# Performance work log

Hardware: AMD Instinct MI355X
Metric: run time of the kernel (lower is better)

Reference implementation:

```python
import jax, jax.numpy as jnp
import numpy as np

GROUP_SIZE = 128
INTERMEDIATE = 18944


def _unpack_int4(packed):
    # packed: [rows, cols//8] int32, 8 nibbles per int32 along output dim
    shifts = jnp.arange(8, dtype=jnp.int32) * 4
    nib = (packed[:, :, None] >> shifts) & 15  # [rows, cols//8, 8]
    return nib.reshape(packed.shape[0], packed.shape[1] * 8)


def awq_gemm(x, qweight, qzeros, scales, group_size):
    # Dequantize: W[i,j] = (w4[i,j] - z4[i//g, j]) * scales[i//g, j]
    w = _unpack_int4(qweight).astype(jnp.float32)           # [in, out]
    z = _unpack_int4(qzeros).astype(jnp.float32)            # [in//g, out]
    s = scales.astype(jnp.float32)                          # [in//g, out]
    W = ((w - jnp.repeat(z, group_size, axis=0)) * jnp.repeat(s, group_size, axis=0))
    return (x @ W.astype(x.dtype))                          # [tokens, out]


def setup_inputs() -> dict:
    key = jax.random.key(0)
    ks = jax.random.split(key, 7)
    imax = 2147483647
    return {
        "x": (jax.random.normal(ks[0], (4096, 3584), dtype=jnp.float32) * 0.02).astype(jnp.float16),
        "qweight_gu": jax.random.randint(ks[1], (3584, 4736), 0, imax, dtype=jnp.int32),
        "qzeros_gu": jax.random.randint(ks[2], (28, 4736), 0, imax, dtype=jnp.int32),
        "scales_gu": (jax.random.uniform(ks[3], (28, 37888), dtype=jnp.float32) * 0.01 + 0.001).astype(jnp.float16),
        "qweight_down": jax.random.randint(ks[4], (18944, 448), 0, imax, dtype=jnp.int32),
        "qzeros_down": jax.random.randint(ks[5], (148, 448), 0, imax, dtype=jnp.int32),
        "scales_down": (jax.random.uniform(ks[6], (148, 3584), dtype=jnp.float32) * 0.01 + 0.001).astype(jnp.float16),
    }


def reference(x, qweight_gu, qzeros_gu, scales_gu, qweight_down, qzeros_down, scales_down):
    # Fused gate+up AWQ GEMM (matches forward path after fuse_gate_up())
    gate_up = awq_gemm(x, qweight_gu, qzeros_gu, scales_gu, GROUP_SIZE)  # [T, 2*I]
    gate = gate_up[..., :INTERMEDIATE]
    up = gate_up[..., INTERMEDIATE:]
    intermediate = jax.nn.silu(gate) * up                                # fused SiLU*mul
    down = awq_gemm(intermediate, qweight_down, qzeros_down, scales_down, GROUP_SIZE)
    return down
```

## Files before the change

kernel.cpp:

```cpp
#include <hip/hip_runtime.h>
#include <hip/hip_fp16.h>
#include <stdint.h>

typedef _Float16 half8 __attribute__((ext_vector_type(8)));
typedef _Float16 h2v __attribute__((ext_vector_type(2)));
typedef float f32x4 __attribute__((ext_vector_type(4)));

#define GLD_LDS16(gp, lp)                                                     \
  __builtin_amdgcn_global_load_lds(                                           \
      (const __attribute__((address_space(1))) void*)(gp),                    \
      (__attribute__((address_space(3))) void*)(lp), 16, 0, 0)
#define GLD_LDS4(gp, lp)                                                      \
  __builtin_amdgcn_global_load_lds(                                           \
      (const __attribute__((address_space(1))) void*)(gp),                    \
      (__attribute__((address_space(3))) void*)(lp), 4, 0, 0)

__global__ void xcvt_kernel(const float* __restrict__ in, __half* __restrict__ out) {
  const size_t i = ((size_t)blockIdx.x * 256 + threadIdx.x) * 4;
  float4 v = *(const float4*)(in + i);
  __half2* o = (__half2*)(out + i);
  o[0] = __floats2half2_rn(v.x, v.y);
  o[1] = __floats2half2_rn(v.z, v.w);
}

__global__ void repack_kernel(const int* __restrict__ qw, uint32_t* __restrict__ rp, int P) {
  const int N = P * 8;
  const int n = blockIdx.x * 256 + threadIdx.x;
  const int j8 = n >> 3;
  const int sh = (n & 7) * 4;
  #pragma unroll
  for (int qi = 0; qi < 4; ++qi) {
    const int q = blockIdx.y * 4 + qi;
    const int* src = qw + (size_t)(q * 8) * P + j8;
    uint32_t r = 0;
    #pragma unroll
    for (int t = 0; t < 8; ++t) {
      uint32_t w = ((uint32_t)src[t * P] >> sh) & 15u;
      r |= w << (4 * (t >> 1) + 16 * (t & 1));
    }
    rp[(size_t)q * N + n] = r;
  }
}

__global__ void smz_kernel(const float* __restrict__ sc, const int* __restrict__ qz,
                           uint32_t* __restrict__ smz, int P) {
  const int N = P * 8;
  const int n = blockIdx.x * 256 + threadIdx.x;
  const int g = blockIdx.y;
  uint32_t sbits = __half_as_ushort(__float2half(sc[(size_t)g * N + n]));
  uint32_t z = ((uint32_t)qz[(size_t)g * P + (n >> 3)] >> ((n & 7) * 4)) & 15u;
  uint32_t hz = 0x6400u | z;
  smz[(size_t)g * N + n] = sbits | (hz << 16);
}

union U32H2 { uint32_t u; h2v h; };
__device__ inline h2v bith2(uint32_t u) { U32H2 t; t.u = u; return t.h; }
__device__ inline uint32_t h2bit(h2v h) { U32H2 t; t.h = h; return t.u; }
__device__ inline half8 dequant8(uint32_t p, h2v s, h2v z) {
  union { uint32_t u[4]; half8 v; } r;
  r.u[0] = h2bit((bith2((p & 0x000F000Fu) | 0x64006400u) - z) * s);
  r.u[1] = h2bit((bith2(((p >> 4) & 0x000F000Fu) | 0x64006400u) - z) * s);
  r.u[2] = h2bit((bith2(((p >> 8) & 0x000F000Fu) | 0x64006400u) - z) * s);
  r.u[3] = h2bit((bith2(((p >> 12) & 0x000F000Fu) | 0x64006400u) - z) * s);
  return r.v;
}

template <int KDIM, int NW, int T1OFF, int OW, bool SILU, int BXS>
__global__ __launch_bounds__(512, 2) void awq_gemm_big(const __half* __restrict__ A,
                                                       const uint32_t* __restrict__ RP,
                                                       const uint32_t* __restrict__ SMZ,
                                                       void* __restrict__ OUT) {
  constexpr int ABUF = 256 * 64 * 2;
  constexpr int BBUF = 8 * 256 * 4;
  constexpr int BOFF = 3 * ABUF;
  constexpr int ZOFF = BOFF + 3 * BBUF;
  __shared__ __align__(16) unsigned char smem[ZOFF + 2048];

  const int tid = threadIdx.x;
  const int l = tid & 63;
  const int wv = tid >> 6;
  const int wm = wv >> 2;
  const int wn = wv & 3;
  const int l15 = l & 15;
  const int l4 = l >> 4;
  const int l157 = l15 & 7;

  const int row0 = blockIdx.y * 256;
  const int n0 = blockIdx.x * BXS;

  const __half* asrc[4];
  #pragma unroll
  for (int it = 0; it < 4; ++it) {
    int m = it * 64 + (tid >> 3);
    int cs = tid & 7;
    int kc = cs ^ (m & 7);
    asrc[it] = A + (size_t)(row0 + m) * KDIM + kc * 8;
  }

  const uint32_t* bsrc;
  {
    int qr = tid >> 6;
    int c4 = (tid & 63) * 4;
    int S = ((qr & 1) << 4) | ((qr >> 1) << 2);
    int cS = c4 ^ S;
    int bcol = (cS < 128) ? n0 + cS : n0 + T1OFF + (cS - 128);
    bsrc = RP + (size_t)qr * NW + bcol;
  }

  const uint32_t* zsrc;
  {
    int zc = tid & 255;
    zsrc = SMZ + ((zc < 128) ? n0 + zc : n0 + T1OFF + (zc - 128));
  }

  int chi[4];
  #pragma unroll
  for (int nf = 0; nf < 4; ++nf)
    chi[nf] = (nf >> 1) * 128 + wn * 32 + (nf & 1) * 16 + l15;
  int arow[8];
  #pragma unroll
  for (int mf = 0; mf < 8; ++mf)
    arow[mf] = (wm * 128 + mf * 16 + l15) * 128;

  f32x4 acc[4][8];
  const f32x4 zero4 = {0.f, 0.f, 0.f, 0.f};
  #pragma unroll
  for (int nf = 0; nf < 4; ++nf)
    #pragma unroll
    for (int mf = 0; mf < 8; ++mf) acc[nf][mf] = zero4;

  uint32_t s2[4], z2[4];
  constexpr int NSTEP = KDIM / 64;

  #pragma unroll
  for (int it = 0; it < 4; ++it)
    GLD_LDS16(asrc[it], &smem[it * 8192 + tid * 16]);
  GLD_LDS16(bsrc, &smem[BOFF + tid * 16]);
  GLD_LDS4(zsrc, &smem[ZOFF + (tid & 255) * 4]);
  #pragma unroll
  for (int it = 0; it < 4; ++it)
    GLD_LDS16(asrc[it] + 64, &smem[ABUF + it * 8192 + tid * 16]);
  GLD_LDS16(bsrc + (size_t)8 * NW, &smem[BOFF + BBUF + tid * 16]);

  int cur = 0, stg = 2;
  for (int t = 0; t < NSTEP; ++t) {
    if (t == NSTEP - 1)      asm volatile("s_waitcnt vmcnt(0)" ::: "memory");
    else if (t & 1)          asm volatile("s_waitcnt vmcnt(6)" ::: "memory");
    else                     asm volatile("s_waitcnt vmcnt(5)" ::: "memory");
    __builtin_amdgcn_s_barrier();

    if (t + 2 < NSTEP) {
      #pragma unroll
      for (int it = 0; it < 4; ++it)
        GLD_LDS16(asrc[it] + (size_t)(t + 2) * 64,
                  &smem[stg * ABUF + it * 8192 + tid * 16]);
      GLD_LDS16(bsrc + (size_t)(t + 2) * 8 * NW, &smem[BOFF + stg * BBUF + tid * 16]);
      if (((t + 2) & 1) == 0) {
        const int g = (t + 2) >> 1;
        GLD_LDS4(zsrc + (size_t)g * NW, &smem[ZOFF + (g & 1) * 1024 + (tid & 255) * 4]);
      }
    }

    if ((t & 1) == 0) {
      const uint32_t* zl = (const uint32_t*)&smem[ZOFF + ((t >> 1) & 1) * 1024];
      #pragma unroll
      for (int nf = 0; nf < 4; ++nf) {
        uint32_t u = zl[chi[nf]];
        uint32_t lo = u & 0xFFFFu;
        s2[nf] = lo | (lo << 16);
        z2[nf] = (u & 0xFFFF0000u) | (u >> 16);
      }
    }

    uint32_t bq[2][4];
    const uint32_t* bdw = (const uint32_t*)&smem[BOFF + cur * BBUF];
    #pragma unroll
    for (int kk = 0; kk < 2; ++kk) {
      const int Sl = ((l4 & 1) << 4) | (kk << 3) | ((l4 >> 1) << 2);
      #pragma unroll
      for (int nf = 0; nf < 4; ++nf)
        bq[kk][nf] = bdw[(kk * 4 + l4) * 256 + (chi[nf] ^ Sl)];
    }

    const unsigned char* abase = &smem[cur * ABUF];
    __builtin_amdgcn_s_setprio(1);
    #pragma unroll
    for (int kk = 0; kk < 2; ++kk) {
      const int coff = ((kk * 4 + l4) ^ l157) * 16;
      half8 afr[8];
      #pragma unroll
      for (int mf = 0; mf < 8; ++mf)
        afr[mf] = *(const half8*)&smem[(size_t)(abase - smem) + arow[mf] + coff];
      half8 bfr[4];
      #pragma unroll
      for (int nf = 0; nf < 4; ++nf)
        bfr[nf] = dequant8(bq[kk][nf], bith2(s2[nf]), bith2(z2[nf]));
      #pragma unroll
      for (int nf = 0; nf < 4; ++nf)
        #pragma unroll
        for (int mf = 0; mf < 8; ++mf)
          acc[nf][mf] =
              __builtin_amdgcn_mfma_f32_16x16x32_f16(afr[mf], bfr[nf], acc[nf][mf], 0, 0, 0);
    }
    __builtin_amdgcn_s_setprio(0);

    cur = (cur == 2) ? 0 : cur + 1;
    stg = (stg == 2) ? 0 : stg + 1;
  }

  if (SILU) {
    __half* O = (__half*)OUT;
    #pragma unroll
    for (int nfg = 0; nfg < 2; ++nfg)
      #pragma unroll
      for (int mf = 0; mf < 8; ++mf)
        #pragma unroll
        for (int r = 0; r < 4; ++r) {
          int row = row0 + wm * 128 + mf * 16 + l4 * 4 + r;
          int col = n0 + wn * 32 + nfg * 16 + l15;
          float gf = __half2float(__float2half(acc[nfg][mf][r]));
          float uf = __half2float(__float2half(acc[2 + nfg][mf][r]));
          float sig = 1.f / (1.f + __expf(-gf));
          float sil = __half2float(__float2half(gf * sig));
          O[(size_t)row * OW + col] = __float2half(sil * uf);
        }
  } else {
    float* O = (float*)OUT;
    #pragma unroll
    for (int nf = 0; nf < 4; ++nf)
      #pragma unroll
      for (int mf = 0; mf < 8; ++mf)
        #pragma unroll
        for (int r = 0; r < 4; ++r) {
          int row = row0 + wm * 128 + mf * 16 + l4 * 4 + r;
          int col = n0 + (nf >> 1) * T1OFF + wn * 32 + (nf & 1) * 16 + l15;
          O[(size_t)row * OW + col] = __half2float(__float2half(acc[nf][mf][r]));
        }
  }
}

template <int KDIM, int NW, int T1OFF, int OW, bool SILU, int BXS>
__global__ __launch_bounds__(512, 4) void awq_gemm(const __half* __restrict__ A,
                                                   const uint32_t* __restrict__ RP,
                                                   const uint32_t* __restrict__ SMZ,
                                                   void* __restrict__ OUT) {
  constexpr int ABUF = 128 * 64 * 2;
  constexpr int BBUF = 8 * 256 * 4;
  constexpr int BOFF = 3 * ABUF;
  constexpr int ZOFF = BOFF + 3 * BBUF;
  __shared__ __align__(16) unsigned char smem[ZOFF + 2048];

  const int tid = threadIdx.x;
  const int l = tid & 63;
  const int wv = tid >> 6;
  const int l15 = l & 15;
  const int l4 = l >> 4;
  const int wc = wv * 16;

  const int row0 = blockIdx.y * 128;
  const int n0 = blockIdx.x * BXS;

  const __half* asrc[2];
  #pragma unroll
  for (int it = 0; it < 2; ++it) {
    int m = it * 64 + (tid >> 3);
    int cs = tid & 7;
    int kc = cs ^ (m & 7);
    asrc[it] = A + (size_t)(row0 + m) * KDIM + kc * 8;
  }

  const uint32_t* bsrc;
  {
    int qr = tid >> 6;
    int c4 = (tid & 63) * 4;
    int S = ((qr & 1) << 4) | ((qr >> 1) << 2);
    int cS = c4 ^ S;
    int bcol = (cS < 128) ? n0 + cS : n0 + T1OFF + (cS - 128);
    bsrc = RP + (size_t)qr * NW + bcol;
  }

  const uint32_t* zsrc;
  {
    int w3 = wv & 3;
    int zc = w3 * 64 + l;
    zsrc = SMZ + ((zc < 128) ? n0 + zc : n0 + T1OFF + (zc - 128));
  }
  const int zdst = ZOFF + (wv & 3) * 256;

  f32x4 acc0[8], acc1[8];
  const f32x4 zero4 = {0.f, 0.f, 0.f, 0.f};
  #pragma unroll
  for (int mf = 0; mf < 8; ++mf) { acc0[mf] = zero4; acc1[mf] = zero4; }

  uint32_t s2[2], z2[2];
  constexpr int NSTEP = KDIM / 64;

  #pragma unroll
  for (int it = 0; it < 2; ++it)
    GLD_LDS16(asrc[it], &smem[it * 8192 + tid * 16]);
  GLD_LDS16(bsrc, &smem[BOFF + tid * 16]);
  GLD_LDS4(zsrc, &smem[zdst]);
  #pragma unroll
  for (int it = 0; it < 2; ++it)
    GLD_LDS16(asrc[it] + 64, &smem[ABUF + it * 8192 + tid * 16]);
  GLD_LDS16(bsrc + (size_t)8 * NW, &smem[BOFF + BBUF + tid * 16]);

  int cur = 0, stg = 2;
  for (int t = 0; t < NSTEP; ++t) {
    if (t == NSTEP - 1)      asm volatile("s_waitcnt vmcnt(0)" ::: "memory");
    else if (t & 1)          asm volatile("s_waitcnt vmcnt(4)" ::: "memory");
    else                     asm volatile("s_waitcnt vmcnt(3)" ::: "memory");
    __builtin_amdgcn_s_barrier();

    if (t + 2 < NSTEP) {
      #pragma unroll
      for (int it = 0; it < 2; ++it)
        GLD_LDS16(asrc[it] + (size_t)(t + 2) * 64,
                  &smem[stg * ABUF + it * 8192 + tid * 16]);
      GLD_LDS16(bsrc + (size_t)(t + 2) * 8 * NW, &smem[BOFF + stg * BBUF + tid * 16]);
      if (((t + 2) & 1) == 0) {
        const int g = (t + 2) >> 1;
        GLD_LDS4(zsrc + (size_t)g * NW, &smem[zdst + (g & 1) * 1024]);
      }
    }

    if ((t & 1) == 0) {
      const uint32_t* zl = (const uint32_t*)&smem[ZOFF + ((t >> 1) & 1) * 1024];
      uint32_t u0 = zl[wc + l15];
      uint32_t u1 = zl[128 + wc + l15];
      uint32_t lo0 = u0 & 0xFFFFu, lo1 = u1 & 0xFFFFu;
      s2[0] = lo0 | (lo0 << 16);
      z2[0] = (u0 & 0xFFFF0000u) | (u0 >> 16);
      s2[1] = lo1 | (lo1 << 16);
      z2[1] = (u1 & 0xFFFF0000u) | (u1 >> 16);
    }

    uint32_t bq[2][2];
    const uint32_t* bdw = (const uint32_t*)&smem[BOFF + cur * BBUF];
    #pragma unroll
    for (int kk = 0; kk < 2; ++kk) {
      const int Sl = ((l4 & 1) << 4) | (kk << 3) | ((l4 >> 1) << 2);
      const int qrow = (kk * 4 + l4) * 256;
      bq[kk][0] = bdw[qrow + ((wc + l15) ^ Sl)];
      bq[kk][1] = bdw[qrow + ((128 + wc + l15) ^ Sl)];
    }

    const unsigned char* abase = &smem[cur * ABUF];
    __builtin_amdgcn_s_setprio(1);
    #pragma unroll
    for (int kk = 0; kk < 2; ++kk) {
      half8 b0 = dequant8(bq[kk][0], bith2(s2[0]), bith2(z2[0]));
      half8 b1 = dequant8(bq[kk][1], bith2(s2[1]), bith2(z2[1]));
      const int chunkoff = ((kk * 4 + l4) ^ (l15 & 7)) * 16;
      #pragma unroll
      for (int mf = 0; mf < 8; ++mf) {
        half8 a = *(const half8*)(abase + (mf * 16 + l15) * 128 + chunkoff);
        acc0[mf] = __builtin_amdgcn_mfma_f32_16x16x32_f16(a, b0, acc0[mf], 0, 0, 0);
        acc1[mf] = __builtin_amdgcn_mfma_f32_16x16x32_f16(a, b1, acc1[mf], 0, 0, 0);
      }
    }
    __builtin_amdgcn_s_setprio(0);

    cur = (cur == 2) ? 0 : cur + 1;
    stg = (stg == 2) ? 0 : stg + 1;
  }

  if (SILU) {
    __half* O = (__half*)OUT;
    #pragma unroll
    for (int mf = 0; mf < 8; ++mf)
      #pragma unroll
      for (int r = 0; r < 4; ++r) {
        int row = row0 + mf * 16 + l4 * 4 + r;
        int col = n0 + wc + l15;
        float gf = __half2float(__float2half(acc0[mf][r]));
        float uf = __half2float(__float2half(acc1[mf][r]));
        float sig = 1.f / (1.f + __expf(-gf));
        float sil = __half2float(__float2half(gf * sig));
        O[(size_t)row * OW + col] = __float2half(sil * uf);
      }
  } else {
    float* O = (float*)OUT;
    #pragma unroll
    for (int mf = 0; mf < 8; ++mf)
      #pragma unroll
      for (int r = 0; r < 4; ++r) {
        int row = row0 + mf * 16 + l4 * 4 + r;
        int col0 = n0 + wc + l15;
        int col1 = n0 + T1OFF + wc + l15;
        O[(size_t)row * OW + col0] = __half2float(__float2half(acc0[mf][r]));
        O[(size_t)row * OW + col1] = __half2float(__float2half(acc1[mf][r]));
      }
  }
}

extern "C" void kernel_launch(void* const* d_in, const int* in_sizes, int n_in,
                              void* d_out, int out_size, void* d_ws, size_t ws_size,
                              hipStream_t stream) {
  const float* x_f32 = (const float*)d_in[0];
  const int* qw_gu = (const int*)d_in[1];
  const int* qz_gu = (const int*)d_in[2];
  const float* sc_gu = (const float*)d_in[3];
  const int* qw_dn = (const int*)d_in[4];
  const int* qz_dn = (const int*)d_in[5];
  const float* sc_dn = (const float*)d_in[6];

  char* ws = (char*)d_ws;
  __half* interm   = (__half*)ws;
  uint32_t* rp_gu  = (uint32_t*)(ws + 155189248ull);
  uint32_t* smz_gu = (uint32_t*)(ws + 223084544ull);
  __half* xh       = (__half*)(ws + 227328000ull);
  uint32_t* rp_dn  = (uint32_t*)(ws + 155189248ull);
  uint32_t* smz_dn = (uint32_t*)(ws + 189136896ull);

  xcvt_kernel<<<14336, 256, 0, stream>>>(x_f32, xh);
  repack_kernel<<<dim3(148, 112), 256, 0, stream>>>(qw_gu, rp_gu, 4736);
  smz_kernel<<<dim3(148, 28), 256, 0, stream>>>(sc_gu, qz_gu, smz_gu, 4736);

  awq_gemm_big<3584, 37888, 18944, 18944, true, 128>
      <<<dim3(148, 16), 512, 0, stream>>>(xh, rp_gu, smz_gu, (void*)interm);

  repack_kernel<<<dim3(14, 592), 256, 0, stream>>>(qw_dn, rp_dn, 448);
  smz_kernel<<<dim3(14, 148), 256, 0, stream>>>(sc_dn, qz_dn, smz_dn, 448);

  awq_gemm<18944, 3584, 128, 3584, false, 256>
      <<<dim3(14, 32), 512, 0, stream>>>(interm, rp_dn, smz_dn, d_out);
}
```

Measured before the change: 1.683 ms.

## Interleave global loads, LDS reads and MFMA in four barrier-separated phases

Splits each K-step of the int4 GEMM main loop into four sub-phases. Each phase issues part of the next-stage global-to-LDS prefetch, loads a quarter of the A fragments, dequantizes B, and then runs a block of MFMAs between explicit s_barriers. The goal is to spread memory traffic across the compute phases and keep waves in lockstep, and smaller fragment arrays lower register pressure. The cost is more barriers per iteration and a changed vmcnt accounting scheme, which could stall or create hazards if the counts are wrong.

```diff
diff --git a/kernel.cpp b/kernel.cpp
--- a/kernel.cpp
+++ b/kernel.cpp
@@ -14,6 +14,8 @@
   __builtin_amdgcn_global_load_lds(                                           \
       (const __attribute__((address_space(1))) void*)(gp),                    \
       (__attribute__((address_space(3))) void*)(lp), 4, 0, 0)
+
+#define SBAR() asm volatile("s_barrier" ::: "memory")
 
 __global__ void xcvt_kernel(const float* __restrict__ in, __half* __restrict__ out) {
   const size_t i = ((size_t)blockIdx.x * 256 + threadIdx.x) * 4;
@@ -142,25 +144,24 @@
     GLD_LDS16(asrc[it] + 64, &smem[ABUF + it * 8192 + tid * 16]);
   GLD_LDS16(bsrc + (size_t)8 * NW, &smem[BOFF + BBUF + tid * 16]);
 
+  asm volatile("s_waitcnt vmcnt(5)" ::: "memory");
+  SBAR();
+
   int cur = 0, stg = 2;
   for (int t = 0; t < NSTEP; ++t) {
-    if (t == NSTEP - 1)      asm volatile("s_waitcnt vmcnt(0)" ::: "memory");
-    else if (t & 1)          asm volatile("s_waitcnt vmcnt(6)" ::: "memory");
-    else                     asm volatile("s_waitcnt vmcnt(5)" ::: "memory");
-    __builtin_amdgcn_s_barrier();
+    const int aoff = cur * ABUF;
+    uint32_t bq[4];
+    half8 afr[4], bfr[4];
+    const uint32_t* bdw = (const uint32_t*)&smem[BOFF + cur * BBUF];
+    const int Sl0 = ((l4 & 1) << 4) | ((l4 >> 1) << 2);
 
     if (t + 2 < NSTEP) {
-      #pragma unroll
-      for (int it = 0; it < 4; ++it)
-        GLD_LDS16(asrc[it] + (size_t)(t + 2) * 64,
-                  &smem[stg * ABUF + it * 8192 + tid * 16]);
-      GLD_LDS16(bsrc + (size_t)(t + 2) * 8 * NW, &smem[BOFF + stg * BBUF + tid * 16]);
-      if (((t + 2) & 1) == 0) {
-        const int g = (t + 2) >> 1;
-        GLD_LDS4(zsrc + (size_t)g * NW, &smem[ZOFF + (g & 1) * 1024 + (tid & 255) * 4]);
-      }
-    }
-
+      GLD_LDS16(asrc[0] + (size_t)(t + 2) * 64, &smem[stg * ABUF + tid * 16]);
+      GLD_LDS16(asrc[1] + (size_t)(t + 2) * 64, &smem[stg * ABUF + 8192 + tid * 16]);
+    }
+    #pragma unroll
+    for (int nf = 0; nf < 4; ++nf)
+      bq[nf] = bdw[l4 * 256 + (chi[nf] ^ Sl0)];
     if ((t & 1) == 0) {
       const uint32_t* zl = (const uint32_t*)&smem[ZOFF + ((t >> 1) & 1) * 1024];
       #pragma unroll
@@ -171,38 +172,80 @@
         z2[nf] = (u & 0xFFFF0000u) | (u >> 16);
       }
     }
-
-    uint32_t bq[2][4];
-    const uint32_t* bdw = (const uint32_t*)&smem[BOFF + cur * BBUF];
-    #pragma unroll
-    for (int kk = 0; kk < 2; ++kk) {
-      const int Sl = ((l4 & 1) << 4) | (kk << 3) | ((l4 >> 1) << 2);
-      #pragma unroll
-      for (int nf = 0; nf < 4; ++nf)
-        bq[kk][nf] = bdw[(kk * 4 + l4) * 256 + (chi[nf] ^ Sl)];
-    }
-
-    const unsigned char* abase = &smem[cur * ABUF];
+    #pragma unroll
+    for (int i = 0; i < 4; ++i)
+      afr[i] = *(const half8*)&smem[aoff + arow[i] + (l4 ^ l157) * 16];
+    #pragma unroll
+    for (int nf = 0; nf < 4; ++nf)
+      bfr[nf] = dequant8(bq[nf], bith2(s2[nf]), bith2(z2[nf]));
+    SBAR();
     __builtin_amdgcn_s_setprio(1);
     #pragma unroll
-    for (int kk = 0; kk < 2; ++kk) {
-      const int coff = ((kk * 4 + l4) ^ l157) * 16;
-      half8 afr[8];
-      #pragma unroll
-      for (int mf = 0; mf < 8; ++mf)
-        afr[mf] = *(const half8*)&smem[(size_t)(abase - smem) + arow[mf] + coff];
-      half8 bfr[4];
-      #pragma unroll
-      for (int nf = 0; nf < 4; ++nf)
-        bfr[nf] = dequant8(bq[kk][nf], bith2(s2[nf]), bith2(z2[nf]));
-      #pragma unroll
-      for (int nf = 0; nf < 4; ++nf)
-        #pragma unroll
-        for (int mf = 0; mf < 8; ++mf)
-          acc[nf][mf] =
-              __builtin_amdgcn_mfma_f32_16x16x32_f16(afr[mf], bfr[nf], acc[nf][mf], 0, 0, 0);
-    }
+    for (int nf = 0; nf < 4; ++nf)
+      #pragma unroll
+      for (int i = 0; i < 4; ++i)
+        acc[nf][i] = __builtin_amdgcn_mfma_f32_16x16x32_f16(afr[i], bfr[nf], acc[nf][i], 0, 0, 0);
     __builtin_amdgcn_s_setprio(0);
+    SBAR();
+
+    if (t + 2 < NSTEP) {
+      GLD_LDS16(asrc[2] + (size_t)(t + 2) * 64, &smem[stg * ABUF + 16384 + tid * 16]);
+      GLD_LDS16(asrc[3] + (size_t)(t + 2) * 64, &smem[stg * ABUF + 24576 + tid * 16]);
+    }
+    #pragma unroll
+    for (int i = 0; i < 4; ++i)
+      afr[i] = *(const half8*)&smem[aoff + arow[4 + i] + (l4 ^ l157) * 16];
+    SBAR();
+    __builtin_amdgcn_s_setprio(1);
+    #pragma unroll
+    for (int nf = 0; nf < 4; ++nf)
+      #pragma unroll
+      for (int i = 0; i < 4; ++i)
+        acc[nf][4 + i] = __builtin_amdgcn_mfma_f32_16x16x32_f16(afr[i], bfr[nf], acc[nf][4 + i], 0, 0, 0);
+    __builtin_amdgcn_s_setprio(0);
+    SBAR();
+
+    if (t + 2 < NSTEP) {
+      GLD_LDS16(bsrc + (size_t)(t + 2) * 8 * NW, &smem[BOFF + stg * BBUF + tid * 16]);
+      if (((t + 2) & 1) == 0) {
+        const int g = (t + 2) >> 1;
+        GLD_LDS4(zsrc + (size_t)g * NW, &smem[ZOFF + (g & 1) * 1024 + (tid & 255) * 4]);
+      }
+    }
+    #pragma unroll
+    for (int nf = 0; nf < 4; ++nf)
+      bq[nf] = bdw[(4 + l4) * 256 + (chi[nf] ^ (Sl0 | 8))];
+    #pragma unroll
+    for (int i = 0; i < 4; ++i)
+      afr[i] = *(const half8*)&smem[aoff + arow[i] + ((4 + l4) ^ l157) * 16];
+    #pragma unroll
+    for (int nf = 0; nf < 4; ++nf)
+      bfr[nf] = dequant8(bq[nf], bith2(s2[nf]), bith2(z2[nf]));
+    SBAR();
+    __builtin_amdgcn_s_setprio(1);
+    #pragma unroll
+    for (int nf = 0; nf < 4; ++nf)
+      #pragma unroll
+      for (int i = 0; i < 4; ++i)
+        acc[nf][i] = __builtin_amdgcn_mfma_f32_16x16x32_f16(afr[i], bfr[nf], acc[nf][i], 0, 0, 0);
+    __builtin_amdgcn_s_setprio(0);
+    SBAR();
+
+    #pragma unroll
+    for (int i = 0; i < 4; ++i)
+      afr[i] = *(const half8*)&smem[aoff + arow[4 + i] + ((4 + l4) ^ l157) * 16];
+    SBAR();
+    __builtin_amdgcn_s_setprio(1);
+    #pragma unroll
+    for (int nf = 0; nf < 4; ++nf)
+      #pragma unroll
+      for (int i = 0; i < 4; ++i)
+        acc[nf][4 + i] = __builtin_amdgcn_mfma_f32_16x16x32_f16(afr[i], bfr[nf], acc[nf][4 + i], 0, 0, 0);
+    __builtin_amdgcn_s_setprio(0);
+    if (t + 2 >= NSTEP)      asm volatile("s_waitcnt vmcnt(0)" ::: "memory");
+    else if (t & 1)          asm volatile("s_waitcnt vmcnt(5)" ::: "memory");
+    else                     asm volatile("s_waitcnt vmcnt(6)" ::: "memory");
+    SBAR();
 
     cur = (cur == 2) ? 0 : cur + 1;
     stg = (stg == 2) ? 0 : stg + 1;
```

After: 1.828 ms. 1.09x slower.
